# Optimization experiments

Hardware: AMD Instinct MI355X
Metric: run time of the kernel (lower is better)

Reference implementation:

```python
import jax, jax.numpy as jnp
import numpy as np

ITERS = 10  # resonator iterations (iterations=10 in init_kwargs)

def _bipolar(key, shape):
    return jnp.where(jax.random.normal(key, shape) >= 0, 1.0, -1.0).astype(jnp.float32)

def setup_inputs() -> dict:
    key = jax.random.key(0)
    k1, k2, k3 = jax.random.split(key, 3)
    b, f, v, d = 64, 4, 256, 16384
    input_ = _bipolar(k1, (b, d))
    init_estimates = _bipolar(k2, (b, f, d))
    codebooks = _bipolar(k3, (f, v, d))
    return {"input": input_, "init_estimates": init_estimates, "codebooks": codebooks}

def _sign(x):
    # multiset quantize: bipolar sign (ties -> +1), matching MAP-VSA quantization
    return jnp.where(x >= 0, 1.0, -1.0).astype(x.dtype)

def reference(input, init_estimates, codebooks):
    """CONCURRENT resonator, SOFTWARE mode, activation=NONE, stoch=NONE.
    input: (b, d) bipolar; init_estimates: (b, f, d); codebooks: (f, v, d).
    For bipolar vectors: bind = elementwise *, inverse = identity, so
    multibind of all-but-factor-j equals (product over all f) * estimate_j
    (since e*e = 1). This replaces the roll+stack+multibind with one fused pass.
    """
    def step(est, _):
        total = jnp.prod(est, axis=-2, keepdims=True)        # (b, 1, d)
        inv_others = total * est                             # (b, f, d) product of other factors
        new_est = input[:, None, :] * inv_others             # unbind: (b, f, d)
        sim = jnp.einsum('bfd,fvd->bfv', new_est, codebooks) # dot_similarity
        # multiset(codebook, similarity, quantize=True): sign of similarity-weighted sum
        est_new = _sign(jnp.einsum('bfv,fvd->bfd', sim, codebooks))
        return est_new, None
    est, _ = jax.lax.scan(step, init_estimates, None, length=ITERS)
    # cleanup: argmax of |similarity| per factor (argmax_abs=True)
    sim = jnp.einsum('bfd,fvd->bfv', est, codebooks)
    outcome = jnp.argmax(jnp.abs(sim), axis=-1)              # (b, f) codeword indices
    return est, outcome
```

## Files before the change

### kernel.cpp

```cpp
#include <hip/hip_runtime.h>
#include <stdint.h>

typedef unsigned long long ull;
typedef unsigned short ushort_t;
typedef __attribute__((ext_vector_type(8))) short bf16x8;
typedef __attribute__((ext_vector_type(4))) float f32x4;


__global__ __launch_bounds__(1024) void pack_all(
        const float* __restrict__ in, const float* __restrict__ est_f,
        ull* __restrict__ in_bits, ull* __restrict__ est_bits) {
    int gw   = (int)((blockIdx.x * 1024 + threadIdx.x) >> 6);
    int lane = threadIdx.x & 63;
    if (gw < 16384) {
        float x = in[(size_t)gw * 64 + lane];
        ull m = __ballot(x < 0.0f);
        if (lane == 0) in_bits[gw] = m;
    } else {
        int g = gw - 16384;
        float x = est_f[(size_t)g * 64 + lane];
        ull m = __ballot(x < 0.0f);
        if (lane == 0) est_bits[g] = m;
    }
}

__global__ __launch_bounds__(1024) void pack_cbw(const float* __restrict__ cb, ull* __restrict__ cbw) {
    int gw   = (int)((blockIdx.x * 1024 + threadIdx.x) >> 6);
    int lane = threadIdx.x & 63;
    int w = gw & 255, fv = gw >> 8;
    float x = cb[(size_t)fv * 16384 + (size_t)w * 64 + lane];
    ull m = __ballot(x < 0.0f);
    if (lane == 0) cbw[(size_t)((fv >> 8) * 256 + w) * 256 + (fv & 255)] = m;
}

__global__ __launch_bounds__(1024) void pack_cbT(const ull* __restrict__ cbw, ull* __restrict__ cbT) {
    int gw   = (int)((blockIdx.x * 1024 + threadIdx.x) >> 6);
    int lane = threadIdx.x & 63;
    int f = gw >> 16, rem = gw & 65535, j = rem >> 14, d = rem & 16383;
    ull w = cbw[(size_t)(f * 256 + (d >> 6)) * 256 + j * 64 + lane];
    ull m = __ballot((w >> (d & 63)) & 1ull);
    if (lane == 0) cbT[(size_t)(f * 4 + j) * 16384 + d] = m;
}

__device__ __forceinline__ ushort_t f2bf(int x) {
    return (ushort_t)(__float_as_uint((float)x) >> 16);
}

__global__ __launch_bounds__(1024) void simA_kernel(
        const ull* __restrict__ in_bits, const ull* __restrict__ est_in,
        const ull* __restrict__ cbw, ushort_t* __restrict__ simAB) {
    int bA = blockIdx.x >> 2, fA = blockIdx.x & 3;
    __shared__ ull s_ne[256];
    __shared__ short s_hp[4][256];
    int t = threadIdx.x;
    if (t < 256) {
        ull e0 = est_in[(size_t)(bA * 4 + 0) * 256 + t];
        ull e1 = est_in[(size_t)(bA * 4 + 1) * 256 + t];
        ull e2 = est_in[(size_t)(bA * 4 + 2) * 256 + t];
        ull e3 = est_in[(size_t)(bA * 4 + 3) * 256 + t];
        ull u  = in_bits[(size_t)bA * 256 + t] ^ e0 ^ e1 ^ e2 ^ e3;
        ull ef = (fA == 0) ? e0 : ((fA == 1) ? e1 : ((fA == 2) ? e2 : e3));
        s_ne[t] = u ^ ef;
    }
    __syncthreads();
    {
        int v = t & 255, qr = t >> 8;
        const ull* cw = cbw + (size_t)fA * 65536 + (size_t)(qr * 64) * 256 + v;
        int acc = 0;
        #pragma unroll 16
        for (int w = 0; w < 64; ++w)
            acc += __popcll(s_ne[qr * 64 + w] ^ cw[(size_t)w * 256]);
        s_hp[qr][v] = (short)acc;
    }
    __syncthreads();
    if (t < 256) {
        int q = 16384 - (s_hp[0][t] + s_hp[1][t] + s_hp[2][t] + s_hp[3][t]);
        size_t base = ((size_t)(fA * 64 + bA)) * 512 + t;
        simAB[base]       = f2bf(q >> 8);
        simAB[base + 256] = f2bf(q & 255);
    }
}

__global__ __launch_bounds__(512) void gemm_kernel(
        const ull* __restrict__ cbT, const ushort_t* __restrict__ simAB,
        ull* __restrict__ est_out) {
    int fB = blockIdx.x >> 6, dblk = blockIdx.x & 63;
    __shared__ int4 sB[8192];
    __shared__ ull s_ball[8][8][4];
    __shared__ int s_off[256];
    int t = threadIdx.x, lane = t & 63, wave = t >> 6;

    if (t < 256) {
        int d = dblk * 256 + t;
        int npop = 0;
        #pragma unroll
        for (int j = 0; j < 4; ++j) npop += __popcll(cbT[((size_t)fB * 4 + j) * 16384 + d]);
        s_off[t] = 8192 * (256 - 2 * npop);
    }

    #pragma unroll 4
    for (int it = 0; it < 16; ++it) {
        int flat = it * 512 + t;
        int kc = flat >> 10, nt = (flat >> 6) & 15, l = flat & 63;
        int v0 = kc * 32 + ((l >> 4) << 3);
        int d  = dblk * 256 + nt * 16 + (l & 15);
        ull w = cbT[((size_t)fB * 4 + (v0 >> 6)) * 16384 + d];
        unsigned bits = (unsigned)(w >> (v0 & 63)) & 0xFFu;
        int4 val;
        val.x = 0x3F803F80 | ((bits & 1u) << 15)        | ((bits & 2u) << 30);
        val.y = 0x3F803F80 | (((bits >> 2) & 1u) << 15) | (((bits >> 2) & 2u) << 30);
        val.z = 0x3F803F80 | (((bits >> 4) & 1u) << 15) | (((bits >> 4) & 2u) << 30);
        val.w = 0x3F803F80 | (((bits >> 6) & 1u) << 15) | (((bits >> 6) & 2u) << 30);
        sB[flat] = val;
    }

    int mw = wave & 3, ntb = (wave >> 2) << 3;
    const ushort_t* abase = simAB
        + ((size_t)(fB * 64 + mw * 16 + (lane & 15))) * 512 + ((lane >> 4) << 3);
    bf16x8 Ahi[8], Alo[8];
    #pragma unroll
    for (int kc = 0; kc < 8; ++kc) {
        Ahi[kc] = *(const bf16x8*)(abase + kc * 32);
        Alo[kc] = *(const bf16x8*)(abase + 256 + kc * 32);
    }
    __syncthreads();

    #pragma unroll 2
    for (int ntl = 0; ntl < 8; ++ntl) {
        int nt = ntb + ntl;
        f32x4 acch = {0.f, 0.f, 0.f, 0.f}, accl = {0.f, 0.f, 0.f, 0.f};
        #pragma unroll
        for (int kc = 0; kc < 8; ++kc) {
            bf16x8 B = *(const bf16x8*)&sB[(kc * 16 + nt) * 64 + lane];
            acch = __builtin_amdgcn_mfma_f32_16x16x32_bf16(Ahi[kc], B, acch, 0, 0, 0);
            accl = __builtin_amdgcn_mfma_f32_16x16x32_bf16(Alo[kc], B, accl, 0, 0, 0);
        }
        float offf = (float)s_off[nt * 16 + (lane & 15)];
        #pragma unroll
        for (int r = 0; r < 4; ++r) {
            float S = 256.0f * acch[r] + accl[r];
            ull m = __ballot(S < offf);
            if (lane == 0) s_ball[wave][nt & 7][r] = m;
        }
    }
    __syncthreads();

    if (t < 256) {
        int b = t >> 2, w4 = t & 3;
        int wv = (b >> 4) + ((w4 >= 2) ? 4 : 0);
        ull word = 0;
        #pragma unroll
        for (int k = 0; k < 4; ++k) {
            int nt = w4 * 4 + k;
            ull m = s_ball[wv][nt & 7][b & 3];
            word |= ((m >> (((b >> 2) & 3) * 16)) & 0xFFFFull) << (k * 16);
        }
        est_out[((size_t)(b * 4 + fB)) * 256 + dblk * 4 + w4] = word;
    }
}

__global__ __launch_bounds__(1024) void final_kernel(
        const ull* __restrict__ est, const ull* __restrict__ cbw, float* __restrict__ out) {
    int b = blockIdx.x >> 2, f = blockIdx.x & 3;
    __shared__ ull s_e[256];
    __shared__ short s_hp[4][256];
    __shared__ int s_sim[256];
    int t = threadIdx.x;
    if (t < 256) s_e[t] = est[(size_t)(b * 4 + f) * 256 + t];
    __syncthreads();
    {
        int v = t & 255, qr = t >> 8;
        const ull* cw = cbw + (size_t)f * 65536 + (size_t)(qr * 64) * 256 + v;
        int acc = 0;
        #pragma unroll 16
        for (int w = 0; w < 64; ++w)
            acc += __popcll(s_e[qr * 64 + w] ^ cw[(size_t)w * 256]);
        s_hp[qr][v] = (short)acc;
    }
    __syncthreads();
    if (t < 256) {
        int h = s_hp[0][t] + s_hp[1][t] + s_hp[2][t] + s_hp[3][t];
        s_sim[t] = 16384 - 2 * h;
    }
    __syncthreads();
    int wv = t >> 6, lane = t & 63;
    if (wv == 0) {
        int best_a = -1, best_v = 0;
        #pragma unroll
        for (int c = 0; c < 4; ++c) {
            int v = c * 64 + lane;
            int sv = s_sim[v];
            int a = sv < 0 ? -sv : sv;
            if (a > best_a) { best_a = a; best_v = v; }
        }
        #pragma unroll
        for (int off = 1; off < 64; off <<= 1) {
            int oa = __shfl_xor(best_a, off);
            int ov = __shfl_xor(best_v, off);
            if (oa > best_a || (oa == best_a && ov < best_v)) { best_a = oa; best_v = ov; }
        }
        if (lane == 0) out[4194304 + b * 4 + f] = (float)best_v;
    }
    #pragma unroll
    for (int i = 0; i < 16; ++i) {
        int d = i * 1024 + t;
        ull w = s_e[d >> 6];
        out[((size_t)(b * 4 + f) << 14) + d] = ((w >> (d & 63)) & 1ull) ? -1.0f : 1.0f;
    }
}

extern "C" void kernel_launch(void* const* d_in, const int* in_sizes, int n_in,
                              void* d_out, int out_size, void* d_ws, size_t ws_size,
                              hipStream_t stream) {
    const float* input    = (const float*)d_in[0];
    const float* init_est = (const float*)d_in[1];
    const float* cb       = (const float*)d_in[2];
    float* out = (float*)d_out;
    char* ws = (char*)d_ws;

    ull* in_bits    = (ull*)(ws + 0);
    ull* est0       = (ull*)(ws + 131072);
    ull* est1       = (ull*)(ws + 655360);
    ull* cbw        = (ull*)(ws + 1179648);
    ull* cbT        = (ull*)(ws + 3276800);
    ushort_t* simAB = (ushort_t*)(ws + 5373952);

    pack_all<<<5120, 1024, 0, stream>>>(input, init_est, in_bits, est0);
    pack_cbw<<<16384, 1024, 0, stream>>>(cb, cbw);
    pack_cbT<<<16384, 1024, 0, stream>>>(cbw, cbT);

    ull* bufs[2] = { est0, est1 };
    for (int i = 0; i < 10; ++i) {
        simA_kernel<<<256, 1024, 0, stream>>>(in_bits, bufs[i & 1], cbw, simAB);
        gemm_kernel<<<256, 512, 0, stream>>>(cbT, simAB, bufs[(i & 1) ^ 1]);
    }
    final_kernel<<<256, 1024, 0, stream>>>(est0, cbw, out);
}
```

Before: 378.2 us.

## Tile similarity kernel over batch and codeword blocks, fuse pack kernels, split final

```diff
diff --git a/kernel.cpp b/kernel.cpp
--- a/kernel.cpp
+++ b/kernel.cpp
@@ -7,30 +7,28 @@
 typedef __attribute__((ext_vector_type(4))) float f32x4;
 
 
-__global__ __launch_bounds__(1024) void pack_all(
+__global__ __launch_bounds__(1024) void pack_mega(
         const float* __restrict__ in, const float* __restrict__ est_f,
-        ull* __restrict__ in_bits, ull* __restrict__ est_bits) {
+        const float* __restrict__ cb,
+        ull* __restrict__ in_bits, ull* __restrict__ est_bits, ull* __restrict__ cbw) {
     int gw   = (int)((blockIdx.x * 1024 + threadIdx.x) >> 6);
     int lane = threadIdx.x & 63;
     if (gw < 16384) {
         float x = in[(size_t)gw * 64 + lane];
         ull m = __ballot(x < 0.0f);
         if (lane == 0) in_bits[gw] = m;
-    } else {
+    } else if (gw < 81920) {
         int g = gw - 16384;
         float x = est_f[(size_t)g * 64 + lane];
         ull m = __ballot(x < 0.0f);
         if (lane == 0) est_bits[g] = m;
-    }
-}
-
-__global__ __launch_bounds__(1024) void pack_cbw(const float* __restrict__ cb, ull* __restrict__ cbw) {
-    int gw   = (int)((blockIdx.x * 1024 + threadIdx.x) >> 6);
-    int lane = threadIdx.x & 63;
-    int w = gw & 255, fv = gw >> 8;
-    float x = cb[(size_t)fv * 16384 + (size_t)w * 64 + lane];
-    ull m = __ballot(x < 0.0f);
-    if (lane == 0) cbw[(size_t)((fv >> 8) * 256 + w) * 256 + (fv & 255)] = m;
+    } else {
+        int g = gw - 81920;
+        int w = g & 255, fv = g >> 8;
+        float x = cb[(size_t)fv * 16384 + (size_t)w * 64 + lane];
+        ull m = __ballot(x < 0.0f);
+        if (lane == 0) cbw[(size_t)((fv >> 8) * 256 + w) * 256 + (fv & 255)] = m;
+    }
 }
 
 __global__ __launch_bounds__(1024) void pack_cbT(const ull* __restrict__ cbw, ull* __restrict__ cbT) {
@@ -46,45 +44,74 @@
     return (ushort_t)(__float_as_uint((float)x) >> 16);
 }
 
-__global__ __launch_bounds__(1024) void simA_kernel(
+__global__ __launch_bounds__(1024) void simA2_kernel(
         const ull* __restrict__ in_bits, const ull* __restrict__ est_in,
-        const ull* __restrict__ cbw, ushort_t* __restrict__ simAB) {
-    int bA = blockIdx.x >> 2, fA = blockIdx.x & 3;
-    __shared__ ull s_ne[256];
-    __shared__ short s_hp[4][256];
+        const ull* __restrict__ cbw, ushort_t* __restrict__ outq, int mode) {
+    int bid = blockIdx.x;
+    int f    = (bid & 7) >> 1;
+    int sub  = (bid & 1) * 32 + (bid >> 3);
+    int vblk = sub & 3, bblk = sub >> 2;
+
+    __shared__ ull s_cw[64][257];
+    __shared__ ull s_ne[4][257];
+    __shared__ short s_p[4][4][64];
+
     int t = threadIdx.x;
+
+    {
+        int bl = t >> 8, w = t & 255;
+        int b = bblk * 4 + bl;
+        ull e0 = est_in[(size_t)(b * 4 + 0) * 256 + w];
+        ull e1 = est_in[(size_t)(b * 4 + 1) * 256 + w];
+        ull e2 = est_in[(size_t)(b * 4 + 2) * 256 + w];
+        ull e3 = est_in[(size_t)(b * 4 + 3) * 256 + w];
+        ull ef = (f == 0) ? e0 : ((f == 1) ? e1 : ((f == 2) ? e2 : e3));
+        ull val = mode ? ef
+                       : (in_bits[(size_t)b * 256 + w] ^ e0 ^ e1 ^ e2 ^ e3 ^ ef);
+        s_ne[bl][w] = val;
+    }
+    #pragma unroll 4
+    for (int i = 0; i < 16; ++i) {
+        int idx = i * 1024 + t;
+        int v = idx & 63, w = idx >> 6;
+        s_cw[v][w] = cbw[(size_t)(f * 256 + w) * 256 + vblk * 64 + v];
+    }
+    __syncthreads();
+
+    {
+        int lane = t & 63, wave = t >> 6;
+        int bi = wave & 3, q = wave >> 2;
+        int acc0 = 0, acc1 = 0;
+        #pragma unroll 8
+        for (int w = q * 64; w < q * 64 + 64; w += 2) {
+            acc0 += __popcll(s_ne[bi][w]     ^ s_cw[lane][w]);
+            acc1 += __popcll(s_ne[bi][w + 1] ^ s_cw[lane][w + 1]);
+        }
+        s_p[bi][q][lane] = (short)(acc0 + acc1);
+    }
+    __syncthreads();
+
     if (t < 256) {
-        ull e0 = est_in[(size_t)(bA * 4 + 0) * 256 + t];
-        ull e1 = est_in[(size_t)(bA * 4 + 1) * 256 + t];
-        ull e2 = est_in[(size_t)(bA * 4 + 2) * 256 + t];
-        ull e3 = est_in[(size_t)(bA * 4 + 3) * 256 + t];
-        ull u  = in_bits[(size_t)bA * 256 + t] ^ e0 ^ e1 ^ e2 ^ e3;
-        ull ef = (fA == 0) ? e0 : ((fA == 1) ? e1 : ((fA == 2) ? e2 : e3));
-        s_ne[t] = u ^ ef;
-    }
-    __syncthreads();
-    {
-        int v = t & 255, qr = t >> 8;
-        const ull* cw = cbw + (size_t)fA * 65536 + (size_t)(qr * 64) * 256 + v;
-        int acc = 0;
-        #pragma unroll 16
-        for (int w = 0; w < 64; ++w)
-            acc += __popcll(s_ne[qr * 64 + w] ^ cw[(size_t)w * 256]);
-        s_hp[qr][v] = (short)acc;
-    }
-    __syncthreads();
-    if (t < 256) {
-        int q = 16384 - (s_hp[0][t] + s_hp[1][t] + s_hp[2][t] + s_hp[3][t]);
-        size_t base = ((size_t)(fA * 64 + bA)) * 512 + t;
-        simAB[base]       = f2bf(q >> 8);
-        simAB[base + 256] = f2bf(q & 255);
+        int bi = t >> 6, v2 = t & 63;
+        int h = s_p[bi][0][v2] + s_p[bi][1][v2] + s_p[bi][2][v2] + s_p[bi][3][v2];
+        int q16 = 16384 - h;
+        int b = bblk * 4 + bi, v = vblk * 64 + v2;
+        if (mode == 0) {
+            size_t base = ((size_t)(f * 64 + b)) * 512 + v;
+            outq[base]       = f2bf(q16 >> 8);
+            outq[base + 256] = f2bf(q16 & 255);
+        } else {
+            outq[((size_t)(f * 64 + b)) * 256 + v] = (ushort_t)q16;
+        }
     }
 }
 
 __global__ __launch_bounds__(512) void gemm_kernel(
         const ull* __restrict__ cbT, const ushort_t* __restrict__ simAB,
         ull* __restrict__ est_out) {
-    int fB = blockIdx.x >> 6, dblk = blockIdx.x & 63;
+    int bid = blockIdx.x;
+    int fB   = (bid & 7) >> 1;
+    int dblk = (bid & 1) * 32 + (bid >> 3);
     __shared__ int4 sB[8192];
     __shared__ ull s_ball[8][8][4];
     __shared__ int s_off[256];
@@ -159,39 +186,19 @@
     }
 }
 
-__global__ __launch_bounds__(1024) void final_kernel(
-        const ull* __restrict__ est, const ull* __restrict__ cbw, float* __restrict__ out) {
-    int b = blockIdx.x >> 2, f = blockIdx.x & 3;
-    __shared__ ull s_e[256];
-    __shared__ short s_hp[4][256];
-    __shared__ int s_sim[256];
+__global__ __launch_bounds__(256) void final2_kernel(
+        const ull* __restrict__ est, const ushort_t* __restrict__ simF,
+        float* __restrict__ out) {
     int t = threadIdx.x;
-    if (t < 256) s_e[t] = est[(size_t)(b * 4 + f) * 256 + t];
-    __syncthreads();
-    {
-        int v = t & 255, qr = t >> 8;
-        const ull* cw = cbw + (size_t)f * 65536 + (size_t)(qr * 64) * 256 + v;
-        int acc = 0;
-        #pragma unroll 16
-        for (int w = 0; w < 64; ++w)
-            acc += __popcll(s_e[qr * 64 + w] ^ cw[(size_t)w * 256]);
-        s_hp[qr][v] = (short)acc;
-    }
-    __syncthreads();
-    if (t < 256) {
-        int h = s_hp[0][t] + s_hp[1][t] + s_hp[2][t] + s_hp[3][t];
-        s_sim[t] = 16384 - 2 * h;
-    }
-    __syncthreads();
-    int wv = t >> 6, lane = t & 63;
-    if (wv == 0) {
+    if (blockIdx.x < 256 && t < 64) {
+        int b = blockIdx.x >> 2, f = blockIdx.x & 3;
+        const ushort_t* sf = simF + ((size_t)(f * 64 + b)) * 256 + t * 4;
         int best_a = -1, best_v = 0;
         #pragma unroll
-        for (int c = 0; c < 4; ++c) {
-            int v = c * 64 + lane;
-            int sv = s_sim[v];
-            int a = sv < 0 ? -sv : sv;
-            if (a > best_a) { best_a = a; best_v = v; }
+        for (int k = 0; k < 4; ++k) {
+            int sim = 2 * (int)sf[k] - 16384;
+            int a = sim < 0 ? -sim : sim;
+            if (a > best_a) { best_a = a; best_v = t * 4 + k; }
         }
         #pragma unroll
         for (int off = 1; off < 64; off <<= 1) {
@@ -199,14 +206,22 @@
             int ov = __shfl_xor(best_v, off);
             if (oa > best_a || (oa == best_a && ov < best_v)) { best_a = oa; best_v = ov; }
         }
-        if (lane == 0) out[4194304 + b * 4 + f] = (float)best_v;
-    }
-    #pragma unroll
-    for (int i = 0; i < 16; ++i) {
-        int d = i * 1024 + t;
-        ull w = s_e[d >> 6];
-        out[((size_t)(b * 4 + f) << 14) + d] = ((w >> (d & 63)) & 1ull) ? -1.0f : 1.0f;
-    }
+        if (t == 0) out[4194304 + b * 4 + f] = (float)best_v;
+    }
+    int flat = blockIdx.x * 2048 + t * 8;
+    ull w = est[flat >> 6];
+    unsigned bits = (unsigned)(w >> (flat & 63)) & 0xFFu;
+    float4 lo, hi;
+    lo.x = (bits & 1u)   ? -1.0f : 1.0f;
+    lo.y = (bits & 2u)   ? -1.0f : 1.0f;
+    lo.z = (bits & 4u)   ? -1.0f : 1.0f;
+    lo.w = (bits & 8u)   ? -1.0f : 1.0f;
+    hi.x = (bits & 16u)  ? -1.0f : 1.0f;
+    hi.y = (bits & 32u)  ? -1.0f : 1.0f;
+    hi.z = (bits & 64u)  ? -1.0f : 1.0f;
+    hi.w = (bits & 128u) ? -1.0f : 1.0f;
+    *(float4*)(out + flat)     = lo;
+    *(float4*)(out + flat + 4) = hi;
 }
 
 extern "C" void kernel_launch(void* const* d_in, const int* in_sizes, int n_in,
@@ -224,15 +239,16 @@
     ull* cbw        = (ull*)(ws + 1179648);
     ull* cbT        = (ull*)(ws + 3276800);
     ushort_t* simAB = (ushort_t*)(ws + 5373952);
-
-    pack_all<<<5120, 1024, 0, stream>>>(input, init_est, in_bits, est0);
-    pack_cbw<<<16384, 1024, 0, stream>>>(cb, cbw);
+    ushort_t* simF  = simAB;
+
+    pack_mega<<<21504, 1024, 0, stream>>>(input, init_est, cb, in_bits, est0, cbw);
     pack_cbT<<<16384, 1024, 0, stream>>>(cbw, cbT);
 
     ull* bufs[2] = { est0, est1 };
     for (int i = 0; i < 10; ++i) {
-        simA_kernel<<<256, 1024, 0, stream>>>(in_bits, bufs[i & 1], cbw, simAB);
+        simA2_kernel<<<256, 1024, 0, stream>>>(in_bits, bufs[i & 1], cbw, simAB, 0);
         gemm_kernel<<<256, 512, 0, stream>>>(cbT, simAB, bufs[(i & 1) ^ 1]);
     }
-    final_kernel<<<256, 1024, 0, stream>>>(est0, cbw, out);
-}
+    simA2_kernel<<<256, 1024, 0, stream>>>(in_bits, est0, cbw, simF, 1);
+    final2_kernel<<<2048, 256, 0, stream>>>(est0, simF, out);
+}
```

Result: faster. 363.4 us (-3.9%).
